# Performance work log

Measured on AMD Instinct MI355X. Metric: run time of the kernel, lower is better.

Reference implementation:

```python
import jax, jax.numpy as jnp
import numpy as np

B, T, I, H = 128, 256, 512, 1024


def setup_inputs() -> dict:
    key = jax.random.key(0)
    ks = jax.random.split(key, 16)
    s_in = 1.0 / np.sqrt(I)
    s_h = 1.0 / np.sqrt(H)
    d = {
        "x": jax.random.normal(ks[0], (B, T, I), jnp.float32),
        "x_d": jax.random.normal(ks[1], (B, T, I), jnp.float32),
        "hidden": jnp.zeros((B, H), jnp.float32),
        "cell": jnp.zeros((B, H), jnp.float32),
    }
    for j, n in enumerate(["Wii", "Wif", "Wig", "Wio", "Wid", "Wro"]):
        d[n] = (jax.random.normal(ks[2 + j], (H, I), jnp.float32) * s_in)
    for j, n in enumerate(["Whi", "Whf", "Whg", "Who", "Whd"]):
        d[n] = (jax.random.normal(ks[8 + j], (H, H), jnp.float32) * s_h)
    for n in ["bi", "bf", "bg", "bo", "bd", "Wrb"]:
        d[n] = jnp.zeros((H,), jnp.float32)
    return d


def reference(x, x_d, hidden, cell,
              Wii, Whi, bi, Wif, Whf, bf, Wig, Whg, bg,
              Wio, Who, bo, Wid, Whd, bd, Wro, Wrb):
    # Precompute input-to-hidden contributions for all timesteps: (B,T,H)
    pi = jnp.einsum('bti,hi->bth', x, Wii) + bi
    pf = jnp.einsum('bti,hi->bth', x, Wif) + bf
    pg = jnp.einsum('bti,hi->bth', x, Wig) + bg
    po = jnp.einsum('bti,hi->bth', x, Wio) + bo
    pd = jnp.einsum('bti,hi->bth', x_d, Wid) + bd

    def step(carry, inp):
        h, c = carry
        pi_t, pf_t, pg_t, po_t, pd_t = inp  # each (B,H)
        i_t = jax.nn.sigmoid(pi_t + h @ Whi.T)
        f_t = jax.nn.sigmoid(pf_t + h @ Whf.T)
        g_t = jnp.tanh(pg_t + h @ Whg.T)
        o_t = jax.nn.sigmoid(po_t + h @ Who.T)
        d_t = jax.nn.sigmoid(pd_t + h @ Whd.T)
        c_new = f_t * c + i_t * g_t + d_t
        h_new = o_t * jnp.tanh(c_new)
        return (h_new, c_new), h_new

    xs = tuple(jnp.swapaxes(a, 0, 1) for a in (pi, pf, pg, po, pd))  # (T,B,H)
    (h_last, c_last), hs = jax.lax.scan(step, (hidden, cell), xs)
    hs = jnp.swapaxes(hs, 0, 1)  # (B,T,H)

    # Output projection per timestep (original reuses Who for the readout)
    y = jnp.tanh(jnp.einsum('bti,hi->bth', x, Wro)
                 + jnp.einsum('bth,gh->btg', hs, Who) + Wrb)
    return y, h_last, c_last
```

## Files before the change

### kernel.cpp

```cpp
#include <hip/hip_runtime.h>


using bf16x8 = __attribute__((ext_vector_type(8))) __bf16;
using f32x4  = __attribute__((ext_vector_type(4))) float;

#define MFMA16(a, b, c) __builtin_amdgcn_mfma_f32_16x16x32_bf16(a, b, c, 0, 0, 0)

static __device__ __forceinline__ float b2f(ushort u) {
  union { unsigned int i; float f; } v; v.i = ((unsigned int)u) << 16; return v.f;
}
static __device__ __forceinline__ ushort f2b(float f) {
  union { float f; unsigned int i; } v; v.f = f;
  unsigned int x = v.i;
  return (ushort)((x + 0x7fffu + ((x >> 16) & 1u)) >> 16);
}
static __device__ __forceinline__ float sigm(float x) {
  return 1.0f / (1.0f + __expf(-x));
}
static __device__ __forceinline__ float tanhfast(float x) {
  float e = __expf(2.0f * x);
  return 1.0f - 2.0f / (e + 1.0f);
}

static __device__ __forceinline__ void grid_barrier(unsigned int* flags,
                                                    unsigned int gen)
{
  __syncthreads();
  if (threadIdx.x == 0) {
    asm volatile("s_waitcnt vmcnt(0)" ::: "memory");
    __hip_atomic_store(flags + blockIdx.x, gen, __ATOMIC_RELAXED,
                       __HIP_MEMORY_SCOPE_AGENT);
  }
  while (__hip_atomic_load(flags + threadIdx.x, __ATOMIC_RELAXED,
                           __HIP_MEMORY_SCOPE_AGENT) < gen) {
    __builtin_amdgcn_s_sleep(1);
  }
  asm volatile("" ::: "memory");
  __syncthreads();
}

__global__ __launch_bounds__(256) void cvt_kernel(const float* __restrict__ src,
                                                  ushort* __restrict__ dst, int n)
{
  int i = (blockIdx.x * 256 + threadIdx.x) * 4;
  if (i < n) {
    float4 v = *(const float4*)(src + i);
    ushort4 o;
    o.x = f2b(v.x); o.y = f2b(v.y); o.z = f2b(v.z); o.w = f2b(v.w);
    *(ushort4*)(dst + i) = o;
  }
}

static __device__ __forceinline__ void gemm_kloop(
    const ushort* __restrict__ A, int lda,
    const ushort* __restrict__ Bw, int ldb, int K,
    ushort* As, ushort* Bs, f32x4 (&acc)[4][4])
{
  const int tid = threadIdx.x;
  const int l = tid & 63, w = tid >> 6;
  const int wm = (w >> 1) * 64, wn = (w & 1) * 64;
  const int lr = l & 15, quad = l >> 4;
  bf16x8* Asv = (bf16x8*)As;
  bf16x8* Bsv = (bf16x8*)Bs;
  for (int k0 = 0; k0 < K; k0 += 32) {
    __syncthreads();
#pragma unroll
    for (int it = 0; it < 2; ++it) {
      int c = it * 256 + tid;
      int row = c >> 2, seg = c & 3;
      Asv[c] = *(const bf16x8*)(A  + row * lda + k0 + seg * 8);
      Bsv[c] = *(const bf16x8*)(Bw + row * ldb + k0 + seg * 8);
    }
    __syncthreads();
    bf16x8 af[4], bfr[4];
#pragma unroll
    for (int i = 0; i < 4; ++i) af[i]  = Asv[(wm + i * 16 + lr) * 4 + quad];
#pragma unroll
    for (int j = 0; j < 4; ++j) bfr[j] = Bsv[(wn + j * 16 + lr) * 4 + quad];
#pragma unroll
    for (int i = 0; i < 4; ++i)
#pragma unroll
      for (int j = 0; j < 4; ++j)
        acc[i][j] = MFMA16(af[i], bfr[j], acc[i][j]);
  }
}

__global__ __launch_bounds__(256) void gemm_pre(
    const ushort* __restrict__ xb, const ushort* __restrict__ xdb,
    const ushort* __restrict__ Wb,
    const float* __restrict__ bias5, ushort* __restrict__ P,
    int t0, int lc)
{
  __shared__ __align__(16) ushort As[4096], Bs[4096];
  const int m0 = blockIdx.x * 128;
  const int n0 = blockIdx.y * 128;
  const int g = n0 >> 10;
  const ushort* A = (g == 4) ? xdb : xb;
  const ushort* Bw = Wb + g * 524288 + (n0 & 1023) * 512;
  const int cm1 = (1 << lc) - 1;

  const int tid = threadIdx.x;
  const int l = tid & 63, w = tid >> 6;
  const int wm = (w >> 1) * 64, wn = (w & 1) * 64;
  const int lr = l & 15, quad = l >> 4;
  f32x4 acc[4][4] = {};
  bf16x8* Asv = (bf16x8*)As;
  bf16x8* Bsv = (bf16x8*)Bs;

  for (int k0 = 0; k0 < 512; k0 += 32) {
    __syncthreads();
#pragma unroll
    for (int it = 0; it < 2; ++it) {
      int c = it * 256 + tid;
      int row = c >> 2, seg = c & 3;
      int gr = m0 + row;
      int arow = ((gr >> lc) << 8) + t0 + (gr & cm1);
      Asv[c] = *(const bf16x8*)(A  + arow * 512 + k0 + seg * 8);
      Bsv[c] = *(const bf16x8*)(Bw + row  * 512 + k0 + seg * 8);
    }
    __syncthreads();
    bf16x8 af[4], bfr[4];
#pragma unroll
    for (int i = 0; i < 4; ++i) af[i]  = Asv[(wm + i * 16 + lr) * 4 + quad];
#pragma unroll
    for (int j = 0; j < 4; ++j) bfr[j] = Bsv[(wn + j * 16 + lr) * 4 + quad];
#pragma unroll
    for (int i = 0; i < 4; ++i)
#pragma unroll
      for (int j = 0; j < 4; ++j)
        acc[i][j] = MFMA16(af[i], bfr[j], acc[i][j]);
  }

#pragma unroll
  for (int i = 0; i < 4; ++i)
#pragma unroll
    for (int j = 0; j < 4; ++j) {
      int row = m0 + wm + i * 16 + quad * 4;
      int col = n0 + wn + j * 16 + lr;
      float bias = bias5[col];
#pragma unroll
      for (int r = 0; r < 4; ++r)
        P[(row + r) * 5120 + col] = f2b(acc[i][j][r] + bias);
    }
}

__global__ __launch_bounds__(256, 1) void lstm_chunk(
    const ushort* __restrict__ h0,
    float* __restrict__ cbuf, const ushort* __restrict__ Whb,
    const ushort* __restrict__ P, ushort* __restrict__ hs,
    unsigned int* __restrict__ flags, int t0, int nt, int lc)
{
  __shared__ __align__(16) ushort Bs0[32 * 64 * 8];
  __shared__ __align__(16) ushort Bs1[32 * 64 * 8];
  __shared__ float Pls[128 * 21];
  __shared__ float cs[128 * 5];

  const int tid = threadIdx.x;
  const int l = tid & 63, w = tid >> 6;
  const int lr = l & 15, quad = l >> 4;
  const int nb = blockIdx.x;

  {
    const ushort* wp = Whb + (((lr >> 2) << 10) + nb * 4 + (lr & 3)) * 1024 + quad * 8;
#pragma unroll
    for (int kk = 0; kk < 8; ++kk) {
      int k = w * 8 + kk;
      *(bf16x8*)(Bs0 + (k * 64 + l) * 8) = *(const bf16x8*)(wp + k * 32);
    }
  }
  {
    const ushort* wp = Whb + (4096 + nb * 4 + (lr & 3)) * 1024 + quad * 8;
#pragma unroll
    for (int kk = 0; kk < 8; ++kk) {
      int k = w * 8 + kk;
      bf16x8 v = {};
      if (lr < 4) v = *(const bf16x8*)(wp + k * 32);
      *(bf16x8*)(Bs1 + (k * 64 + l) * 8) = v;
    }
  }
  if (tid < 128) {
    float4 cv = *(const float4*)(cbuf + tid * 1024 + nb * 4);
    cs[tid * 5 + 0] = cv.x; cs[tid * 5 + 1] = cv.y;
    cs[tid * 5 + 2] = cv.z; cs[tid * 5 + 3] = cv.w;
  }
  __syncthreads();

  const bf16x8* B0v = (const bf16x8*)Bs0;
  const bf16x8* B1v = (const bf16x8*)Bs1;

  for (int tt = 0; tt < nt; ++tt) {
    const int t = t0 + tt;
    const ushort* base;
    int rs;
    if (t == 0) { base = h0;                 rs = 1024;   }
    else        { base = hs + (t - 1) * 1024; rs = 262144; }
    const ushort* a0p = base + (w * 32 + lr) * rs + quad * 8;
    const ushort* a1p = a0p + 16 * rs;

    ushort4 p0, p1, p2, p3, p4;
    if (tid < 128) {
      const int prow = ((tid << lc) + tt) * 5120 + nb * 4;
      p0 = *(const ushort4*)(P + prow);
      p1 = *(const ushort4*)(P + prow + 1024);
      p2 = *(const ushort4*)(P + prow + 2048);
      p3 = *(const ushort4*)(P + prow + 3072);
      p4 = *(const ushort4*)(P + prow + 4096);
    }

    f32x4 acc[2][2] = {};
#pragma unroll
    for (int k = 0; k < 32; ++k) {
      bf16x8 a0 = *(const bf16x8*)(a0p + k * 32);
      bf16x8 a1 = *(const bf16x8*)(a1p + k * 32);
      bf16x8 b0 = B0v[k * 64 + l];
      bf16x8 b1 = B1v[k * 64 + l];
      acc[0][0] = MFMA16(a0, b0, acc[0][0]);
      acc[1][0] = MFMA16(a1, b0, acc[1][0]);
      acc[0][1] = MFMA16(a0, b1, acc[0][1]);
      acc[1][1] = MFMA16(a1, b1, acc[1][1]);
    }

#pragma unroll
    for (int i = 0; i < 2; ++i) {
      int b = w * 32 + i * 16 + quad * 4;
#pragma unroll
      for (int r = 0; r < 4; ++r)
        Pls[(b + r) * 21 + lr] = acc[i][0][r];
      if (lr < 4) {
#pragma unroll
        for (int r = 0; r < 4; ++r)
          Pls[(b + r) * 21 + 16 + lr] = acc[i][1][r];
      }
    }
    __syncthreads();

    if (tid < 128) {
      const int b = tid;
      const float* pr = Pls + b * 21;
      ushort hv0, hv1, hv2, hv3;
#pragma unroll
      for (int hc = 0; hc < 4; ++hc) {
        float pi = b2f(((const ushort*)&p0)[hc]) + pr[0 + hc];
        float pf = b2f(((const ushort*)&p1)[hc]) + pr[4 + hc];
        float pg = b2f(((const ushort*)&p2)[hc]) + pr[8 + hc];
        float po = b2f(((const ushort*)&p3)[hc]) + pr[12 + hc];
        float pd = b2f(((const ushort*)&p4)[hc]) + pr[16 + hc];
        float ig = sigm(pi), fg = sigm(pf), gg = tanhfast(pg);
        float og = sigm(po), dg = sigm(pd);
        float cnew = fg * cs[b * 5 + hc] + ig * gg + dg;
        cs[b * 5 + hc] = cnew;
        ushort hb16 = f2b(og * tanhfast(cnew));
        if (hc == 0) hv0 = hb16; else if (hc == 1) hv1 = hb16;
        else if (hc == 2) hv2 = hb16; else hv3 = hb16;
      }
      union { ushort4 s; unsigned long long u; } hu;
      hu.s.x = hv0; hu.s.y = hv1; hu.s.z = hv2; hu.s.w = hv3;
      __hip_atomic_store((unsigned long long*)(hs + (b * 256 + t) * 1024 + nb * 4),
                         hu.u, __ATOMIC_RELAXED, __HIP_MEMORY_SCOPE_AGENT);
    }

    if (tt + 1 < nt)
      grid_barrier(flags, (unsigned int)(t + 1));
  }

  if (tid < 128) {
    float4 cv;
    cv.x = cs[tid * 5 + 0]; cv.y = cs[tid * 5 + 1];
    cv.z = cs[tid * 5 + 2]; cv.w = cs[tid * 5 + 3];
    *(float4*)(cbuf + tid * 1024 + nb * 4) = cv;
  }
}

__global__ __launch_bounds__(64) void lstm_step(
    const ushort* __restrict__ h0, float* __restrict__ cbuf,
    const ushort* __restrict__ Whb, const ushort* __restrict__ P,
    ushort* __restrict__ hs, int t, int tloc, int lc)
{
  const int l = threadIdx.x;
  const int m0 = blockIdx.x * 32;
  const int hc = blockIdx.y * 16;
  const int lr = l & 15, quad = l >> 4;

  const ushort* base;
  int rs;
  if (t == 0) { base = h0;                 rs = 1024;   }
  else        { base = hs + (t - 1) * 1024; rs = 262144; }

  f32x4 acc[2][5] = {};
  const ushort* a0p = base + (m0 + lr) * rs + quad * 8;
  const ushort* a1p = a0p + 16 * rs;
  const ushort* wp = Whb + (hc + lr) * 1024 + quad * 8;

#pragma unroll 2
  for (int k0 = 0; k0 < 1024; k0 += 32) {
    bf16x8 a0 = *(const bf16x8*)(a0p + k0);
    bf16x8 a1 = *(const bf16x8*)(a1p + k0);
    bf16x8 b0 = *(const bf16x8*)(wp + k0);
    bf16x8 b1 = *(const bf16x8*)(wp + 1048576 + k0);
    bf16x8 b2 = *(const bf16x8*)(wp + 2097152 + k0);
    bf16x8 b3 = *(const bf16x8*)(wp + 3145728 + k0);
    bf16x8 b4 = *(const bf16x8*)(wp + 4194304 + k0);
    acc[0][0] = MFMA16(a0, b0, acc[0][0]);
    acc[1][0] = MFMA16(a1, b0, acc[1][0]);
    acc[0][1] = MFMA16(a0, b1, acc[0][1]);
    acc[1][1] = MFMA16(a1, b1, acc[1][1]);
    acc[0][2] = MFMA16(a0, b2, acc[0][2]);
    acc[1][2] = MFMA16(a1, b2, acc[1][2]);
    acc[0][3] = MFMA16(a0, b3, acc[0][3]);
    acc[1][3] = MFMA16(a1, b3, acc[1][3]);
    acc[0][4] = MFMA16(a0, b4, acc[0][4]);
    acc[1][4] = MFMA16(a1, b4, acc[1][4]);
  }

  const int h = hc + lr;
#pragma unroll
  for (int i = 0; i < 2; ++i) {
#pragma unroll
    for (int r = 0; r < 4; ++r) {
      int b = m0 + i * 16 + quad * 4 + r;
      int prow = ((b << lc) + tloc) * 5120;
      float pi = b2f(P[prow + h])          + acc[i][0][r];
      float pf = b2f(P[prow + 1024 + h])   + acc[i][1][r];
      float pg = b2f(P[prow + 2048 + h])   + acc[i][2][r];
      float po = b2f(P[prow + 3072 + h])   + acc[i][3][r];
      float pd = b2f(P[prow + 4096 + h])   + acc[i][4][r];
      float ig = sigm(pi), fg = sigm(pf), gg = tanhfast(pg);
      float og = sigm(po), dg = sigm(pd);
      float cold = cbuf[b * 1024 + h];
      float cnew = fg * cold + ig * gg + dg;
      cbuf[b * 1024 + h] = cnew;
      hs[(b * 256 + t) * 1024 + h] = f2b(og * tanhfast(cnew));
    }
  }
}

__global__ __launch_bounds__(256) void gemm_post(
    const ushort* __restrict__ xb, const ushort* __restrict__ hs,
    const ushort* __restrict__ Wrob, const ushort* __restrict__ Whob,
    const float* __restrict__ Wrb, float* __restrict__ y)
{
  __shared__ __align__(16) ushort As[4096], Bs[4096];
  const int m0 = blockIdx.x * 128;
  const int n0 = blockIdx.y * 128;
  f32x4 acc[4][4] = {};
  gemm_kloop(xb + m0 * 512,  512,  Wrob + n0 * 512,  512,  512,  As, Bs, acc);
  gemm_kloop(hs + m0 * 1024, 1024, Whob + n0 * 1024, 1024, 1024, As, Bs, acc);

  const int tid = threadIdx.x;
  const int l = tid & 63, w = tid >> 6;
  const int wm = (w >> 1) * 64, wn = (w & 1) * 64;
  const int lr = l & 15, quad = l >> 4;
#pragma unroll
  for (int i = 0; i < 4; ++i)
#pragma unroll
    for (int j = 0; j < 4; ++j) {
      int row = m0 + wm + i * 16 + quad * 4;
      int col = n0 + wn + j * 16 + lr;
      float bias = Wrb[col];
#pragma unroll
      for (int r = 0; r < 4; ++r)
        y[(row + r) * 1024 + col] = tanhfast(acc[i][j][r] + bias);
    }
}

__global__ __launch_bounds__(256) void finish_kernel(
    const ushort* __restrict__ hs, const float* __restrict__ cbuf,
    float* __restrict__ out_tail)
{
  int i = blockIdx.x * 256 + threadIdx.x;
  if (i < 131072) {
    int b = i >> 10, h = i & 1023;
    out_tail[i] = b2f(hs[(b * 256 + 255) * 1024 + h]);
    out_tail[131072 + i] = cbuf[i];
  }
}

extern "C" void kernel_launch(void* const* d_in, const int* in_sizes, int n_in,
                              void* d_out, int out_size, void* d_ws, size_t ws_size,
                              hipStream_t stream)
{
  const float* x   = (const float*)d_in[0];
  const float* xd  = (const float*)d_in[1];
  const float* hid = (const float*)d_in[2];
  const float* cel = (const float*)d_in[3];
  const float* Win[6] = {(const float*)d_in[4], (const float*)d_in[5],
                         (const float*)d_in[6], (const float*)d_in[7],
                         (const float*)d_in[8], (const float*)d_in[9]};
  const float* Whn[5] = {(const float*)d_in[10], (const float*)d_in[11],
                         (const float*)d_in[12], (const float*)d_in[13],
                         (const float*)d_in[14]};
  const float* bia[5] = {(const float*)d_in[15], (const float*)d_in[16],
                         (const float*)d_in[17], (const float*)d_in[18],
                         (const float*)d_in[19]};
  const float* Wrb = (const float*)d_in[20];
  float* y = (float*)d_out;

  char* ws = (char*)d_ws;
  ushort* xb    = (ushort*)(ws);
  ushort* xdb   = (ushort*)(ws + 33554432);
  ushort* Wb    = (ushort*)(ws + 67108864);
  ushort* Whb   = (ushort*)(ws + 73400320);
  ushort* hs    = (ushort*)(ws + 83886080);
  ushort* h0    = (ushort*)(ws + 150994944);
  float*  cbuf  = (float*) (ws + 151519232);
  float*  bias5 = (float*) (ws + 152043520);
  unsigned int* flags = (unsigned int*)(ws + 152064000);
  ushort* P     = (ushort*)(ws + 152068096);

  int chunk = 1;
  for (int c = 256; c >= 1; c >>= 1)
    if (152068096ull + (unsigned long long)c * 1310720ull <= (unsigned long long)ws_size) {
      chunk = c; break;
    }
  int lc = 31 - __builtin_clz((unsigned)chunk);

  cvt_kernel<<<16384, 256, 0, stream>>>(x,  xb,  16777216);
  cvt_kernel<<<16384, 256, 0, stream>>>(xd, xdb, 16777216);
  for (int i = 0; i < 6; ++i)
    cvt_kernel<<<512, 256, 0, stream>>>(Win[i], Wb + i * 524288, 524288);
  for (int i = 0; i < 5; ++i)
    cvt_kernel<<<1024, 256, 0, stream>>>(Whn[i], Whb + i * 1048576, 1048576);
  cvt_kernel<<<128, 256, 0, stream>>>(hid, h0, 131072);
  hipMemcpyAsync(cbuf, cel, 131072 * 4, hipMemcpyDeviceToDevice, stream);
  for (int i = 0; i < 5; ++i)
    hipMemcpyAsync(bias5 + i * 1024, bia[i], 4096, hipMemcpyDeviceToDevice, stream);
  hipMemsetAsync(flags, 0, 4096, stream);

  int t = 0;
  bool coop_ok = true;
  for (int c = 0; c < 256 / chunk; ++c) {
    gemm_pre<<<dim3(chunk, 40), 256, 0, stream>>>(xb, xdb, Wb, bias5, P,
                                                  c * chunk, lc);
    if (coop_ok) {
      int t0 = c * chunk;
      void* args[] = {&h0, &cbuf, &Whb, &P, &hs, &flags, &t0, &chunk, &lc};
      hipError_t e = hipLaunchCooperativeKernel((const void*)lstm_chunk,
                                                dim3(256), dim3(256),
                                                args, 0, stream);
      if (e == hipSuccess) {
        t += chunk;
        continue;
      }
      coop_ok = false;
    }
    for (int tt = 0; tt < chunk; ++tt, ++t)
      lstm_step<<<dim3(4, 64), 64, 0, stream>>>(h0, cbuf, Whb, P, hs,
                                                t, tt, lc);
  }
  gemm_post<<<dim3(256, 8), 256, 0, stream>>>(xb, hs, Wb + 5 * 524288,
                                              Whb + 3 * 1048576, Wrb, y);
  finish_kernel<<<512, 256, 0, stream>>>(hs, cbuf, y + 33554432);
}
```

Before: 4.804 ms.

## Use centralized grid barrier with release flag and prefetch next-step preactivations

The all-to-all grid barrier, where every block polled all 256 per-block flags, is replaced by a centralized one. Block 0 gathers the arrival flags with one wavefront and publishes a single release word that all other blocks spin on. While a block waits, it now prefetches the next timestep's precomputed gate inputs from P. The gate nonlinearity work is also spread across all 256 threads, two hidden units each, instead of 128 threads with four each. This trades heavy polling traffic for an extra hop through block 0, and it adds float2 LDS accesses at indices that may be odd.

```diff
diff --git a/kernel.cpp b/kernel.cpp
--- a/kernel.cpp
+++ b/kernel.cpp
@@ -20,23 +20,6 @@
 static __device__ __forceinline__ float tanhfast(float x) {
   float e = __expf(2.0f * x);
   return 1.0f - 2.0f / (e + 1.0f);
-}
-
-static __device__ __forceinline__ void grid_barrier(unsigned int* flags,
-                                                    unsigned int gen)
-{
-  __syncthreads();
-  if (threadIdx.x == 0) {
-    asm volatile("s_waitcnt vmcnt(0)" ::: "memory");
-    __hip_atomic_store(flags + blockIdx.x, gen, __ATOMIC_RELAXED,
-                       __HIP_MEMORY_SCOPE_AGENT);
-  }
-  while (__hip_atomic_load(flags + threadIdx.x, __ATOMIC_RELAXED,
-                           __HIP_MEMORY_SCOPE_AGENT) < gen) {
-    __builtin_amdgcn_s_sleep(1);
-  }
-  asm volatile("" ::: "memory");
-  __syncthreads();
 }
 
 __global__ __launch_bounds__(256) void cvt_kernel(const float* __restrict__ src,
@@ -148,7 +131,8 @@
     const ushort* __restrict__ h0,
     float* __restrict__ cbuf, const ushort* __restrict__ Whb,
     const ushort* __restrict__ P, ushort* __restrict__ hs,
-    unsigned int* __restrict__ flags, int t0, int nt, int lc)
+    unsigned int* __restrict__ flags, unsigned int* __restrict__ release,
+    int t0, int nt, int lc)
 {
   __shared__ __align__(16) ushort Bs0[32 * 64 * 8];
   __shared__ __align__(16) ushort Bs1[32 * 64 * 8];
@@ -187,6 +171,19 @@
 
   const bf16x8* B0v = (const bf16x8*)Bs0;
   const bf16x8* B1v = (const bf16x8*)Bs1;
+
+  const int eb = tid >> 1;
+  const int hp = (tid & 1) * 2;
+
+  ushort2 q0, q1, q2, q3, q4;
+  {
+    const int prow = ((eb << lc) + 0) * 5120 + nb * 4 + hp;
+    q0 = *(const ushort2*)(P + prow);
+    q1 = *(const ushort2*)(P + prow + 1024);
+    q2 = *(const ushort2*)(P + prow + 2048);
+    q3 = *(const ushort2*)(P + prow + 3072);
+    q4 = *(const ushort2*)(P + prow + 4096);
+  }
 
   for (int tt = 0; tt < nt; ++tt) {
     const int t = t0 + tt;
@@ -196,16 +193,6 @@
     else        { base = hs + (t - 1) * 1024; rs = 262144; }
     const ushort* a0p = base + (w * 32 + lr) * rs + quad * 8;
     const ushort* a1p = a0p + 16 * rs;
-
-    ushort4 p0, p1, p2, p3, p4;
-    if (tid < 128) {
-      const int prow = ((tid << lc) + tt) * 5120 + nb * 4;
-      p0 = *(const ushort4*)(P + prow);
-      p1 = *(const ushort4*)(P + prow + 1024);
-      p2 = *(const ushort4*)(P + prow + 2048);
-      p3 = *(const ushort4*)(P + prow + 3072);
-      p4 = *(const ushort4*)(P + prow + 4096);
-    }
 
     f32x4 acc[2][2] = {};
 #pragma unroll
@@ -234,41 +221,69 @@
     }
     __syncthreads();
 
-    if (tid < 128) {
-      const int b = tid;
-      const float* pr = Pls + b * 21;
-      ushort hv0, hv1, hv2, hv3;
-#pragma unroll
-      for (int hc = 0; hc < 4; ++hc) {
-        float pi = b2f(((const ushort*)&p0)[hc]) + pr[0 + hc];
-        float pf = b2f(((const ushort*)&p1)[hc]) + pr[4 + hc];
-        float pg = b2f(((const ushort*)&p2)[hc]) + pr[8 + hc];
-        float po = b2f(((const ushort*)&p3)[hc]) + pr[12 + hc];
-        float pd = b2f(((const ushort*)&p4)[hc]) + pr[16 + hc];
-        float ig = sigm(pi), fg = sigm(pf), gg = tanhfast(pg);
-        float og = sigm(po), dg = sigm(pd);
-        float cnew = fg * cs[b * 5 + hc] + ig * gg + dg;
-        cs[b * 5 + hc] = cnew;
-        ushort hb16 = f2b(og * tanhfast(cnew));
-        if (hc == 0) hv0 = hb16; else if (hc == 1) hv1 = hb16;
-        else if (hc == 2) hv2 = hb16; else hv3 = hb16;
-      }
-      union { ushort4 s; unsigned long long u; } hu;
-      hu.s.x = hv0; hu.s.y = hv1; hu.s.z = hv2; hu.s.w = hv3;
-      __hip_atomic_store((unsigned long long*)(hs + (b * 256 + t) * 1024 + nb * 4),
-                         hu.u, __ATOMIC_RELAXED, __HIP_MEMORY_SCOPE_AGENT);
-    }
-
-    if (tt + 1 < nt)
-      grid_barrier(flags, (unsigned int)(t + 1));
-  }
-
-  if (tid < 128) {
-    float4 cv;
-    cv.x = cs[tid * 5 + 0]; cv.y = cs[tid * 5 + 1];
-    cv.z = cs[tid * 5 + 2]; cv.w = cs[tid * 5 + 3];
-    *(float4*)(cbuf + tid * 1024 + nb * 4) = cv;
-  }
+    {
+      const float* pr = Pls + eb * 21;
+      float pi0 = b2f(q0.x) + pr[0 + hp],  pi1 = b2f(q0.y) + pr[1 + hp];
+      float pf0 = b2f(q1.x) + pr[4 + hp],  pf1 = b2f(q1.y) + pr[5 + hp];
+      float pg0 = b2f(q2.x) + pr[8 + hp],  pg1 = b2f(q2.y) + pr[9 + hp];
+      float po0 = b2f(q3.x) + pr[12 + hp], po1 = b2f(q3.y) + pr[13 + hp];
+      float pd0 = b2f(q4.x) + pr[16 + hp], pd1 = b2f(q4.y) + pr[17 + hp];
+      float c0 = cs[eb * 5 + hp], c1 = cs[eb * 5 + hp + 1];
+      float cn0 = sigm(pf0) * c0 + sigm(pi0) * tanhfast(pg0) + sigm(pd0);
+      float cn1 = sigm(pf1) * c1 + sigm(pi1) * tanhfast(pg1) + sigm(pd1);
+      cs[eb * 5 + hp] = cn0;
+      cs[eb * 5 + hp + 1] = cn1;
+      union { ushort2 s; unsigned int u; } hu;
+      hu.s.x = f2b(sigm(po0) * tanhfast(cn0));
+      hu.s.y = f2b(sigm(po1) * tanhfast(cn1));
+      __hip_atomic_store(
+          (unsigned int*)(hs + (eb * 256 + t) * 1024 + nb * 4 + hp),
+          hu.u, __ATOMIC_RELAXED, __HIP_MEMORY_SCOPE_AGENT);
+    }
+
+    if (tt + 1 < nt) {
+      const unsigned int g = (unsigned int)(t + 1);
+      __syncthreads();
+      if (tid == 0) {
+        asm volatile("s_waitcnt vmcnt(0)" ::: "memory");
+        __hip_atomic_store(flags + nb, g, __ATOMIC_RELAXED,
+                           __HIP_MEMORY_SCOPE_AGENT);
+      }
+      {
+        const int prow = ((eb << lc) + tt + 1) * 5120 + nb * 4 + hp;
+        q0 = *(const ushort2*)(P + prow);
+        q1 = *(const ushort2*)(P + prow + 1024);
+        q2 = *(const ushort2*)(P + prow + 2048);
+        q3 = *(const ushort2*)(P + prow + 3072);
+        q4 = *(const ushort2*)(P + prow + 4096);
+      }
+      if (nb == 0 && tid < 64) {
+        for (;;) {
+          unsigned int f0 = __hip_atomic_load(flags + tid * 4 + 0,
+                              __ATOMIC_RELAXED, __HIP_MEMORY_SCOPE_AGENT);
+          unsigned int f1 = __hip_atomic_load(flags + tid * 4 + 1,
+                              __ATOMIC_RELAXED, __HIP_MEMORY_SCOPE_AGENT);
+          unsigned int f2 = __hip_atomic_load(flags + tid * 4 + 2,
+                              __ATOMIC_RELAXED, __HIP_MEMORY_SCOPE_AGENT);
+          unsigned int f3 = __hip_atomic_load(flags + tid * 4 + 3,
+                              __ATOMIC_RELAXED, __HIP_MEMORY_SCOPE_AGENT);
+          bool ok = (f0 >= g) & (f1 >= g) & (f2 >= g) & (f3 >= g);
+          if (__all(ok)) break;
+          __builtin_amdgcn_s_sleep(1);
+        }
+        if (tid == 0)
+          __hip_atomic_store(release, g, __ATOMIC_RELAXED,
+                             __HIP_MEMORY_SCOPE_AGENT);
+      }
+      while (__hip_atomic_load(release, __ATOMIC_RELAXED,
+                               __HIP_MEMORY_SCOPE_AGENT) < g) {
+        __builtin_amdgcn_s_sleep(1);
+      }
+      asm volatile("" ::: "memory");
+    }
+  }
+
+  *(float2*)(cbuf + eb * 1024 + nb * 4 + hp) = *(float2*)(cs + eb * 5 + hp);
 }
 
 __global__ __launch_bounds__(64) void lstm_step(
@@ -405,6 +420,7 @@
   float*  cbuf  = (float*) (ws + 151519232);
   float*  bias5 = (float*) (ws + 152043520);
   unsigned int* flags = (unsigned int*)(ws + 152064000);
+  unsigned int* release = flags + 512;
   ushort* P     = (ushort*)(ws + 152068096);
 
   int chunk = 1;
@@ -433,7 +449,8 @@
                                                   c * chunk, lc);
     if (coop_ok) {
       int t0 = c * chunk;
-      void* args[] = {&h0, &cbuf, &Whb, &P, &hs, &flags, &t0, &chunk, &lc};
+      void* args[] = {&h0, &cbuf, &Whb, &P, &hs, &flags, &release,
+                      &t0, &chunk, &lc};
       hipError_t e = hipLaunchCooperativeKernel((const void*)lstm_chunk,
                                                 dim3(256), dim3(256),
                                                 args, 0, stream);
```

Measured after the change: 3.988 ms. 1.2x faster.
